# Kernel tuning notes

Measured on AMD Instinct MI355X. Metric: run time of the kernel, lower is better.

Reference implementation:

```python
import jax, jax.numpy as jnp
import numpy as np

BATCH_SIZE = 4096
D = 128
TEMPERATURE = 0.5
EPS = 1e-8  # torch CosineSimilarity eps


def _neg_indices(batch_size):
    # flat indices of the (N, N-2) negative entries: all but diagonal and the +/-B pair
    N = 2 * batch_size
    mask = np.ones((N, N), dtype=bool)
    np.fill_diagonal(mask, False)
    i = np.arange(batch_size)
    mask[i, batch_size + i] = False
    mask[batch_size + i, i] = False
    return np.where(mask.ravel())[0]


NEG_IDX = jnp.asarray(_neg_indices(BATCH_SIZE))


def setup_inputs() -> dict:
    key = jax.random.key(0)
    k1, k2 = jax.random.split(key)
    return {
        "z_i": jax.random.normal(k1, (BATCH_SIZE, D), dtype=jnp.float32),
        "z_j": jax.random.normal(k2, (BATCH_SIZE, D), dtype=jnp.float32),
    }


def reference(z_i, z_j):
    batch_size = z_i.shape[0]
    N = 2 * batch_size
    z = jnp.concatenate([z_i, z_j], axis=0)                       # [N, D]
    norm = jnp.maximum(jnp.linalg.norm(z, axis=1, keepdims=True), EPS)
    zn = z / norm
    sim = (zn @ zn.T) / TEMPERATURE                               # [N, N] cosine sim / temp
    # positives: diagonals at offset +/- batch_size
    pos = jnp.concatenate(
        [jnp.diagonal(sim, offset=batch_size), jnp.diagonal(sim, offset=-batch_size)],
        axis=0,
    )                                                             # [N]
    neg = sim.ravel()[NEG_IDX].reshape(N, N - 2)                  # masked gather
    logits = jnp.concatenate([pos[:, None], neg], axis=1)         # [N, N-1], label = 0
    # CrossEntropyLoss(reduction='sum') with labels all 0, then / N
    loss = jnp.sum(jax.nn.logsumexp(logits, axis=1) - logits[:, 0]) / N
    return loss
```

## Files before the change

kernel.cpp:

```cpp
#include <hip/hip_runtime.h>
#include <hip/hip_bf16.h>


#define BATCH 4096
#define N_TOT 8192
#define DIM 128
#define ROWS_PER_WAVE 32
#define WAVES_PER_BLK 8
#define ROWS_PER_BLK 256
#define NGRP 32
#define NPAIR ((NGRP * (NGRP + 1)) / 2)
#define TILE_C 64
#define NT 4

#define C_LOG2E2 2.8853900817779268f

using bf16x8 = __attribute__((ext_vector_type(8))) __bf16;
using f32x4  = __attribute__((ext_vector_type(4))) float;

typedef __attribute__((address_space(1))) const void cg_void;
typedef __attribute__((address_space(3))) void lds_void;
__device__ __forceinline__ void gll16(const void* g, void* l) {
    __builtin_amdgcn_global_load_lds((cg_void*)g, (lds_void*)l, 16, 0, 0);
}

__global__ __launch_bounds__(256) void k_normalize(const float* __restrict__ zi,
                                                   const float* __restrict__ zj,
                                                   __hip_bfloat16* __restrict__ zn) {
    int row  = blockIdx.x * 4 + (threadIdx.x >> 6);
    int lane = threadIdx.x & 63;
    const float* src = (row < BATCH) ? (zi + (size_t)row * DIM)
                                     : (zj + (size_t)(row - BATCH) * DIM);
    float2 v = ((const float2*)src)[lane];
    float ss = v.x * v.x + v.y * v.y;
    #pragma unroll
    for (int m = 1; m < 64; m <<= 1) ss += __shfl_xor(ss, m);
    float inv = 1.0f / fmaxf(sqrtf(ss), 1e-8f);
    __hip_bfloat162 o;
    o.x = __float2bfloat16(v.x * inv);
    o.y = __float2bfloat16(v.y * inv);
    ((__hip_bfloat162*)(zn + (size_t)row * DIM))[lane] = o;
}

__global__ __launch_bounds__(512, 4) void k_main(const __hip_bfloat16* __restrict__ zn_,
                                                 float* __restrict__ S_contrib) {
    __shared__ __align__(16) char Bs[2][TILE_C * 256];
    __shared__ float colred[WAVES_PER_BLK][ROWS_PER_BLK];

    const int tid  = threadIdx.x;
    const int lane = tid & 63;
    const int wv   = tid >> 6;
    const int l15  = lane & 15;
    const int lb   = lane >> 4;

    int I = 0, rem = blockIdx.x;
    while (rem >= NGRP - I) { rem -= NGRP - I; ++I; }
    const int J = I + rem;
    const bool isdiag = (I == J);

    const int wr0 = I * ROWS_PER_BLK + wv * ROWS_PER_WAVE;
    const int cs0 = J * ROWS_PER_BLK;

    const __bf16* zn = (const __bf16*)zn_;

    bf16x8 a_[2][4];
    #pragma unroll
    for (int g = 0; g < 2; ++g) {
        const __bf16* p = zn + (size_t)(wr0 + g * 16 + l15) * DIM + lb * 8;
        #pragma unroll
        for (int s = 0; s < 4; ++s)
            a_[g][s] = *(const bf16x8*)(p + s * 32);
    }

    ((float4*)colred)[tid] = float4{0.f, 0.f, 0.f, 0.f};

    const char* gB = (const char*)(zn + (size_t)cs0 * DIM);
    int srcoff[2];
    #pragma unroll
    for (int i = 0; i < 2; ++i) {
        int m = i * 512 + tid;
        int c = m >> 4, slot = m & 15;
        int j = slot ^ (c & 7);
        srcoff[i] = c * 256 + j * 16;
    }

    auto STAGE = [&](int t) {
        const char* src = gB + (size_t)t * (TILE_C * 256);
        char* dst = Bs[t & 1];
        #pragma unroll
        for (int i = 0; i < 2; ++i)
            gll16(src + srcoff[i], dst + i * 8192 + wv * 1024);
    };

    f32x4 sumexp[2] = {};

    auto COMPUTE = [&](int t) {
        const char* buf = Bs[t & 1];
        const int c0t = cs0 + t * TILE_C;
        const bool diagtile = ((unsigned)(wr0 - c0t) < (unsigned)TILE_C);
        #pragma unroll
        for (int cb = 0; cb < 4; ++cb) {
            const int c = cb * 16 + l15;
            const char* pc = buf + c * 256;
            bf16x8 b[4];
            #pragma unroll
            for (int s = 0; s < 4; ++s)
                b[s] = *(const bf16x8*)(pc + ((lb + s * 4) ^ (c & 7)) * 16);
            f32x4 acc[2] = {};
            #pragma unroll
            for (int g = 0; g < 2; ++g)
                #pragma unroll
                for (int s = 0; s < 4; ++s)
                    acc[g] = __builtin_amdgcn_mfma_f32_16x16x32_bf16(a_[g][s], b[s], acc[g], 0, 0, 0);
            const int mycol = c0t + c;
            if (diagtile) {
                #pragma unroll
                for (int g = 0; g < 2; ++g)
                    #pragma unroll
                    for (int v = 0; v < 4; ++v) {
                        float e = __builtin_amdgcn_exp2f(acc[g][v] * C_LOG2E2);
                        int row = wr0 + g * 16 + lb * 4 + v;
                        sumexp[g][v] += (mycol == row) ? 0.0f : e;
                    }
            } else {
                float cs = 0.0f;
                #pragma unroll
                for (int g = 0; g < 2; ++g)
                    #pragma unroll
                    for (int v = 0; v < 4; ++v) {
                        float e = __builtin_amdgcn_exp2f(acc[g][v] * C_LOG2E2);
                        sumexp[g][v] += e;
                        cs += e;
                    }
                if (!isdiag) {
                    cs += __shfl_xor(cs, 16);
                    cs += __shfl_xor(cs, 32);
                    if (lb == 0)
                        colred[wv][t * TILE_C + cb * 16 + l15] += cs;
                }
            }
        }
    };

    STAGE(0);
    __syncthreads();
    #pragma unroll
    for (int t = 0; t < NT; ++t) {
        if (t + 1 < NT) STAGE(t + 1);
        COMPUTE(t);
        if (t + 1 < NT) __syncthreads();
    }

    #pragma unroll
    for (int m = 1; m <= 8; m <<= 1)
        #pragma unroll
        for (int g = 0; g < 2; ++g)
            #pragma unroll
            for (int v = 0; v < 4; ++v)
                sumexp[g][v] += __shfl_xor(sumexp[g][v], m);

    if (l15 == 0) {
        #pragma unroll
        for (int g = 0; g < 2; ++g) {
            int row = wr0 + g * 16 + lb * 4;
            *(f32x4*)&S_contrib[(size_t)J * N_TOT + row] = sumexp[g];
        }
    }

    if (!isdiag) {
        __syncthreads();
        if (tid < ROWS_PER_BLK) {
            float s = 0.0f;
            #pragma unroll
            for (int w = 0; w < WAVES_PER_BLK; ++w) s += colred[w][tid];
            S_contrib[(size_t)I * N_TOT + cs0 + tid] = s;
        }
    }
}

__device__ inline float bdot(unsigned a, unsigned b) {
    float alo = __uint_as_float(a << 16), ahi = __uint_as_float(a & 0xffff0000u);
    float blo = __uint_as_float(b << 16), bhi = __uint_as_float(b & 0xffff0000u);
    return fmaf(alo, blo, ahi * bhi);
}

__global__ __launch_bounds__(256) void k_rowsum(const float* __restrict__ S_contrib,
                                                const __hip_bfloat16* __restrict__ zn_,
                                                float* __restrict__ blk_out) {
    const int r = blockIdx.x * 256 + threadIdx.x;
    float S = 0.0f;
    #pragma unroll
    for (int s = 0; s < NGRP; ++s) S += S_contrib[(size_t)s * N_TOT + r];

    const uint4* pa = (const uint4*)((const __bf16*)zn_ + (size_t)r * DIM);
    const uint4* pb = (const uint4*)((const __bf16*)zn_ + (size_t)(r ^ BATCH) * DIM);
    float dot = 0.0f;
    #pragma unroll
    for (int c = 0; c < DIM / 8; ++c) {
        uint4 ua = pa[c], ub = pb[c];
        dot += bdot(ua.x, ub.x) + bdot(ua.y, ub.y) + bdot(ua.z, ub.z) + bdot(ua.w, ub.w);
    }

    float contrib = __logf(S) - 2.0f * dot;

    #pragma unroll
    for (int m = 1; m < 64; m <<= 1) contrib += __shfl_xor(contrib, m);
    __shared__ float sm[4];
    if ((threadIdx.x & 63) == 0) sm[threadIdx.x >> 6] = contrib;
    __syncthreads();
    if (threadIdx.x == 0) blk_out[blockIdx.x] = sm[0] + sm[1] + sm[2] + sm[3];
}

__global__ void k_final(const float* __restrict__ blk_out, float* __restrict__ out) {
    float v = (threadIdx.x < NGRP) ? blk_out[threadIdx.x] : 0.0f;
    #pragma unroll
    for (int m = 1; m < 64; m <<= 1) v += __shfl_xor(v, m);
    if (threadIdx.x == 0) out[0] = v / (float)N_TOT;
}

extern "C" void kernel_launch(void* const* d_in, const int* in_sizes, int n_in,
                              void* d_out, int out_size, void* d_ws, size_t ws_size,
                              hipStream_t stream) {
    const float* zi = (const float*)d_in[0];
    const float* zj = (const float*)d_in[1];
    char* ws = (char*)d_ws;
    __hip_bfloat16* zn = (__hip_bfloat16*)ws;
    float* S_contrib = (float*)(ws + (size_t)2 * 1024 * 1024);
    float* blk       = (float*)(ws + (size_t)3 * 1024 * 1024);
    float* out       = (float*)d_out;

    k_normalize<<<N_TOT / 4, 256, 0, stream>>>(zi, zj, zn);
    k_main<<<NPAIR, 512, 0, stream>>>(zn, S_contrib);
    k_rowsum<<<NGRP, 256, 0, stream>>>(S_contrib, zn, blk);
    k_final<<<1, 64, 0, stream>>>(blk, out);
}
```

Measured before the change: 44.16 us.

## Shrink symmetric tile groups to 128 rows and load whole B tile upfront

Halves the row/column group size to 128, so the triangular pair grid grows from 528 to 2080 blocks of 256 threads, which should improve load balance and occupancy across CUs. Each block now stages its entire 128-column B tile into LDS at once instead of double-buffering four 64-column sub-tiles, which removes the intermediate barriers. Column sums are kept in registers and written to LDS once at the end rather than through per-tile shuffle and LDS updates. The cost is less A-fragment reuse per block, more partial-sum traffic (64 partials per row) for the row-sum kernel to read, and a larger S_contrib workspace region.

```diff
diff --git a/kernel.cpp b/kernel.cpp
--- a/kernel.cpp
+++ b/kernel.cpp
@@ -1,17 +1,18 @@
 #include <hip/hip_runtime.h>
 #include <hip/hip_bf16.h>
+#include <type_traits>
 
 
 #define BATCH 4096
 #define N_TOT 8192
 #define DIM 128
 #define ROWS_PER_WAVE 32
-#define WAVES_PER_BLK 8
-#define ROWS_PER_BLK 256
-#define NGRP 32
+#define WAVES_PER_BLK 4
+#define GRP 128
+#define NGRP 64
 #define NPAIR ((NGRP * (NGRP + 1)) / 2)
 #define TILE_C 64
-#define NT 4
+#define NROWBLK 32
 
 #define C_LOG2E2 2.8853900817779268f
 
@@ -42,10 +43,10 @@
     ((__hip_bfloat162*)(zn + (size_t)row * DIM))[lane] = o;
 }
 
-__global__ __launch_bounds__(512, 4) void k_main(const __hip_bfloat16* __restrict__ zn_,
+__global__ __launch_bounds__(256, 4) void k_main(const __hip_bfloat16* __restrict__ zn_,
                                                  float* __restrict__ S_contrib) {
     __shared__ __align__(16) char Bs[2][TILE_C * 256];
-    __shared__ float colred[WAVES_PER_BLK][ROWS_PER_BLK];
+    __shared__ float colred[WAVES_PER_BLK][GRP];
 
     const int tid  = threadIdx.x;
     const int lane = tid & 63;
@@ -58,8 +59,8 @@
     const int J = I + rem;
     const bool isdiag = (I == J);
 
-    const int wr0 = I * ROWS_PER_BLK + wv * ROWS_PER_WAVE;
-    const int cs0 = J * ROWS_PER_BLK;
+    const int wr0 = I * GRP + wv * ROWS_PER_WAVE;
+    const int cs0 = J * GRP;
 
     const __bf16* zn = (const __bf16*)zn_;
 
@@ -72,30 +73,32 @@
             a_[g][s] = *(const bf16x8*)(p + s * 32);
     }
 
-    ((float4*)colred)[tid] = float4{0.f, 0.f, 0.f, 0.f};
-
     const char* gB = (const char*)(zn + (size_t)cs0 * DIM);
-    int srcoff[2];
-    #pragma unroll
-    for (int i = 0; i < 2; ++i) {
-        int m = i * 512 + tid;
+    int srcoff[4];
+    #pragma unroll
+    for (int i = 0; i < 4; ++i) {
+        int m = (wv * 4 + i) * 64 + lane;
         int c = m >> 4, slot = m & 15;
         int j = slot ^ (c & 7);
         srcoff[i] = c * 256 + j * 16;
     }
 
-    auto STAGE = [&](int t) {
+    #pragma unroll
+    for (int t = 0; t < 2; ++t) {
         const char* src = gB + (size_t)t * (TILE_C * 256);
-        char* dst = Bs[t & 1];
-        #pragma unroll
-        for (int i = 0; i < 2; ++i)
-            gll16(src + srcoff[i], dst + i * 8192 + wv * 1024);
-    };
+        #pragma unroll
+        for (int i = 0; i < 4; ++i)
+            gll16(src + srcoff[i], Bs[t] + (wv * 4 + i) * 1024);
+    }
 
     f32x4 sumexp[2] = {};
-
-    auto COMPUTE = [&](int t) {
-        const char* buf = Bs[t & 1];
+    float csr[8] = {};
+
+    __syncthreads();
+
+    auto COMPUTE = [&](auto tc) {
+        constexpr int t = tc.value;
+        const char* buf = Bs[t];
         const int c0t = cs0 + t * TILE_C;
         const bool diagtile = ((unsigned)(wr0 - c0t) < (unsigned)TILE_C);
         #pragma unroll
@@ -132,24 +135,13 @@
                         sumexp[g][v] += e;
                         cs += e;
                     }
-                if (!isdiag) {
-                    cs += __shfl_xor(cs, 16);
-                    cs += __shfl_xor(cs, 32);
-                    if (lb == 0)
-                        colred[wv][t * TILE_C + cb * 16 + l15] += cs;
-                }
+                csr[t * 4 + cb] += cs;
             }
         }
     };
 
-    STAGE(0);
-    __syncthreads();
-    #pragma unroll
-    for (int t = 0; t < NT; ++t) {
-        if (t + 1 < NT) STAGE(t + 1);
-        COMPUTE(t);
-        if (t + 1 < NT) __syncthreads();
-    }
+    COMPUTE(std::integral_constant<int, 0>{});
+    COMPUTE(std::integral_constant<int, 1>{});
 
     #pragma unroll
     for (int m = 1; m <= 8; m <<= 1)
@@ -168,11 +160,16 @@
     }
 
     if (!isdiag) {
+        #pragma unroll
+        for (int k = 0; k < 8; ++k) {
+            float v = csr[k];
+            v += __shfl_xor(v, 16);
+            v += __shfl_xor(v, 32);
+            if (lb == 0) colred[wv][k * 16 + l15] = v;
+        }
         __syncthreads();
-        if (tid < ROWS_PER_BLK) {
-            float s = 0.0f;
-            #pragma unroll
-            for (int w = 0; w < WAVES_PER_BLK; ++w) s += colred[w][tid];
+        if (tid < GRP) {
+            float s = colred[0][tid] + colred[1][tid] + colred[2][tid] + colred[3][tid];
             S_contrib[(size_t)I * N_TOT + cs0 + tid] = s;
         }
     }
@@ -212,7 +209,7 @@
 }
 
 __global__ void k_final(const float* __restrict__ blk_out, float* __restrict__ out) {
-    float v = (threadIdx.x < NGRP) ? blk_out[threadIdx.x] : 0.0f;
+    float v = (threadIdx.x < NROWBLK) ? blk_out[threadIdx.x] : 0.0f;
     #pragma unroll
     for (int m = 1; m < 64; m <<= 1) v += __shfl_xor(v, m);
     if (threadIdx.x == 0) out[0] = v / (float)N_TOT;
@@ -226,11 +223,11 @@
     char* ws = (char*)d_ws;
     __hip_bfloat16* zn = (__hip_bfloat16*)ws;
     float* S_contrib = (float*)(ws + (size_t)2 * 1024 * 1024);
-    float* blk       = (float*)(ws + (size_t)3 * 1024 * 1024);
+    float* blk       = (float*)(ws + (size_t)4 * 1024 * 1024);
     float* out       = (float*)d_out;
 
     k_normalize<<<N_TOT / 4, 256, 0, stream>>>(zi, zj, zn);
-    k_main<<<NPAIR, 512, 0, stream>>>(zn, S_contrib);
-    k_rowsum<<<NGRP, 256, 0, stream>>>(S_contrib, zn, blk);
+    k_main<<<NPAIR, 256, 0, stream>>>(zn, S_contrib);
+    k_rowsum<<<NROWBLK, 256, 0, stream>>>(S_contrib, zn, blk);
     k_final<<<1, 64, 0, stream>>>(blk, out);
 }
```

Result: faster. 37.55 us (-15.0%).
